# Kernel tuning notes

Hardware: AMD Instinct MI355X
Metric: run time of the kernel (lower is better)

## Reference

```python
import jax, jax.numpy as jnp
import numpy as np

B, N, DIM = 2, 2048, 1024
HEADS, DIM_HEAD = 16, 64
INNER = HEADS * DIM_HEAD  # 1024
SCALE = DIM_HEAD ** -0.5


def setup_inputs() -> dict:
    key = jax.random.key(0)
    ks = jax.random.split(key, 6)
    s = lambda k, shape, fan: jax.random.normal(k, shape, jnp.float32) * (fan ** -0.5)
    return {
        "x": jax.random.normal(ks[0], (B, N, DIM), jnp.float32),
        "similarity": jax.random.normal(ks[1], (B, N), jnp.float32),
        "Wq": s(ks[2], (DIM, INNER), DIM),
        "Wkv": s(ks[3], (DIM, 2 * INNER), DIM),
        "Wo": s(ks[4], (INNER, DIM), INNER),
        "bo": jnp.zeros((DIM,), jnp.float32),
    }


def reference(x, similarity, Wq, Wkv, Wo, bo):
    b, n, _ = x.shape
    h, d = HEADS, DIM_HEAD
    # projections (context = x, self-attention)
    q = (x @ Wq).reshape(b, n, h, d).transpose(0, 2, 1, 3)        # b h n d
    kv = x @ Wkv                                                   # b n 2*inner
    k, v = jnp.split(kv, 2, axis=-1)
    k = k.reshape(b, n, h, d).transpose(0, 2, 1, 3)
    v = v.reshape(b, n, h, d).transpose(0, 2, 1, 3)
    dots = jnp.einsum('bhid,bhjd->bhij', q, k) * SCALE             # b h n n
    # similarity [b,n] -> broadcast as per-query row bias [b,1,n,1]
    dots = dots + similarity[:, None, :, None]
    attn = jax.nn.softmax(dots, axis=-1)
    out = jnp.einsum('bhij,bhjd->bhid', attn, v)                   # b h n d
    out = out.transpose(0, 2, 1, 3).reshape(b, n, h * d)           # b n inner
    return out @ Wo + bo
```

## Files before the change

### kernel.cpp

```cpp
#include <hip/hip_runtime.h>


typedef __attribute__((ext_vector_type(8))) short short8;
typedef __attribute__((ext_vector_type(4))) float float4_;
typedef __attribute__((ext_vector_type(16))) float floatx16;
typedef __attribute__((ext_vector_type(4))) unsigned short ushort4_;
typedef __attribute__((ext_vector_type(4))) unsigned int uint4_;

#define MFMA(a, b, c) __builtin_amdgcn_mfma_f32_16x16x32_bf16((a), (b), (c), 0, 0, 0)
#define MFMA32(a, b, c) __builtin_amdgcn_mfma_f32_32x32x16_bf16((a), (b), (c), 0, 0, 0)

static __device__ __forceinline__ unsigned short f2bf(float f) {
    union { float f; unsigned int u; } v; v.f = f;
    unsigned int r = v.u + 0x7FFFu + ((v.u >> 16) & 1u);
    return (unsigned short)(r >> 16);
}

static __device__ __forceinline__ void gld16(const void* g, void* l) {
    __builtin_amdgcn_global_load_lds(
        (__attribute__((address_space(1))) void*)(g),
        (__attribute__((address_space(3))) void*)(l), 16, 0, 0);
}

__global__ __launch_bounds__(256) void prep(
    const float* __restrict__ X, const float* __restrict__ Wq,
    const float* __restrict__ Wkv, const float* __restrict__ Wo,
    unsigned short* __restrict__ xb, unsigned short* __restrict__ Wt,
    unsigned short* __restrict__ Wot)
{
    const int bid = blockIdx.x, t = threadIdx.x;
    if (bid >= 1024) {
        const int b = bid - 1024;
        const float4_* src = (const float4_*)X;
        ushort4_* dst = (ushort4_*)xb;
        #pragma unroll
        for (int g = 0; g < 8; ++g) {
            const int idx = b * 2048 + g * 256 + t;
            float4_ v = src[idx];
            ushort4_ o;
            o[0] = f2bf(v[0]); o[1] = f2bf(v[1]);
            o[2] = f2bf(v[2]); o[3] = f2bf(v[3]);
            dst[idx] = o;
        }
        return;
    }
    __shared__ float tile[64][65];
    const float* src; unsigned short* dst; int N, kt, nt, drow0;
    if (bid < 256)      { src = Wq;  N = 1024; kt = bid & 15;       nt = bid >> 4;       dst = Wt;  drow0 = nt * 64; }
    else if (bid < 768) { src = Wkv; N = 2048; kt = (bid-256) & 15; nt = (bid-256) >> 4; dst = Wt;  drow0 = 1024 + nt * 64; }
    else                { src = Wo;  N = 1024; kt = (bid-768) & 15; nt = (bid-768) >> 4; dst = Wot; drow0 = nt * 64; }
    const int k0 = kt * 64, n0 = nt * 64;
    const int r0 = t >> 6, c = t & 63;
    #pragma unroll
    for (int i = 0; i < 16; ++i) {
        const int r = i * 4 + r0;
        tile[r][c] = src[(size_t)(k0 + r) * N + n0 + c];
    }
    __syncthreads();
    #pragma unroll
    for (int i = 0; i < 16; ++i) {
        const int rn = i * 4 + r0;
        dst[(size_t)(drow0 + rn) * 1024 + k0 + c] = f2bf(tile[c][rn]);
    }
}

__global__ __launch_bounds__(256) void qkv_gemm2(
    const unsigned short* __restrict__ xb, const unsigned short* __restrict__ Wt,
    unsigned short* __restrict__ q_ws, unsigned short* __restrict__ k_ws,
    unsigned short* __restrict__ vt_ws)
{
    __shared__ unsigned short As[128 * 64];
    __shared__ unsigned short Bs[128 * 64];
    const int t = threadIdx.x, wave = t >> 6, lane = t & 63;
    const int L = lane & 15, quad = lane >> 4;
    const int xcd = blockIdx.x & 7, idx = blockIdx.x >> 3;
    const int mb = (xcd >> 1) * 8 + (idx & 7);
    const int nb = (xcd & 1) * 12 + (idx >> 3);
    const int m0 = mb * 128, n0 = nb * 128;
    const int wr = wave >> 1, wc = wave & 1;

    float4_ z = {0.f, 0.f, 0.f, 0.f};
    float4_ acc[4][4];
    #pragma unroll
    for (int i = 0; i < 4; ++i)
        #pragma unroll
        for (int j = 0; j < 4; ++j) acc[i][j] = z;

    const unsigned short* gA[4]; const unsigned short* gB[4];
    unsigned short* lA[4]; unsigned short* lB[4];
    #pragma unroll
    for (int j = 0; j < 4; ++j) {
        const int cid = wave * 256 + j * 64 + lane;
        const int row = cid >> 3, pc = cid & 7;
        const int lch = pc ^ (row & 7);
        gA[j] = xb + (size_t)(m0 + row) * 1024 + lch * 8;
        gB[j] = Wt + (size_t)(n0 + row) * 1024 + lch * 8;
        lA[j] = As + wave * 2048 + j * 512;
        lB[j] = Bs + wave * 2048 + j * 512;
    }

    for (int kc = 0; kc < 1024; kc += 64) {
        #pragma unroll
        for (int j = 0; j < 4; ++j) {
            gld16(gA[j] + kc, lA[j]);
            gld16(gB[j] + kc, lB[j]);
        }
        __syncthreads();
        #pragma unroll
        for (int ks = 0; ks < 2; ++ks) {
            short8 af[4], bfr[4];
            #pragma unroll
            for (int mt = 0; mt < 4; ++mt) {
                const int rl = wr * 64 + mt * 16 + L;
                af[mt] = *(const short8*)(As + rl * 64 + (((ks * 4 + quad) ^ (L & 7)) << 3));
            }
            #pragma unroll
            for (int nt = 0; nt < 4; ++nt) {
                const int rl = wc * 64 + nt * 16 + L;
                bfr[nt] = *(const short8*)(Bs + rl * 64 + (((ks * 4 + quad) ^ (L & 7)) << 3));
            }
            #pragma unroll
            for (int mt = 0; mt < 4; ++mt)
                #pragma unroll
                for (int nt = 0; nt < 4; ++nt)
                    acc[mt][nt] = MFMA(af[mt], bfr[nt], acc[mt][nt]);
        }
        __syncthreads();
    }

    const int b = m0 >> 11;
    const int type = n0 >> 10;
    #pragma unroll
    for (int mt = 0; mt < 4; ++mt) {
        const int m = (m0 & 2047) + wr * 64 + mt * 16 + quad * 4;
        #pragma unroll
        for (int nt = 0; nt < 4; ++nt) {
            const int cl = (n0 & 1023) + wc * 64 + nt * 16 + L;
            const int h = cl >> 6, d = cl & 63;
            float4_ v = acc[mt][nt];
            if (type == 0) {
                unsigned short* p = q_ws + ((size_t)(b * 16 + h) * 2048 + m) * 64 + d;
                #pragma unroll
                for (int r = 0; r < 4; ++r) p[(size_t)r * 64] = f2bf(v[r] * 0.18033688011f);
            } else if (type == 1) {
                unsigned short* p = k_ws + (size_t)(b * 16 + h) * 131072
                    + (m >> 5) * 2048 + (d >> 3) * 256 + (m & 31) * 8 + (d & 7);
                #pragma unroll
                for (int r = 0; r < 4; ++r) p[r * 8] = f2bf(v[r]);
            } else {
                ushort4_ pk;
                pk[0] = f2bf(v[0]); pk[1] = f2bf(v[1]);
                pk[2] = f2bf(v[2]); pk[3] = f2bf(v[3]);
                *(ushort4_*)(vt_ws + (size_t)(b * 16 + h) * 131072
                    + (m >> 3) * 512 + d * 8 + (m & 7)) = pk;
            }
        }
    }
}

#define LOADT(k0_, k1_, k2_, k3_, v00_, v10_, v01_, v11_, IT) do {            \
    const unsigned short* kp_ = kbase + (IT) * 2048;                          \
    const unsigned short* vp_ = vbase + (IT) * 2048;                          \
    k0_ = *(const short8*)(kp_);        k1_ = *(const short8*)(kp_ + 512);    \
    k2_ = *(const short8*)(kp_ + 1024); k3_ = *(const short8*)(kp_ + 1536);   \
    v00_ = *(const short8*)(vp_);        v10_ = *(const short8*)(vp_ + 1024); \
    v01_ = *(const short8*)(vp_ + 256);  v11_ = *(const short8*)(vp_ + 1280); \
} while (0)

#define COMPT(k0_, k1_, k2_, k3_, v00_, v10_, v01_, v11_) do {                \
    _Pragma("unroll")                                                         \
    for (int qt = 0; qt < 2; ++qt) {                                          \
        floatx16 s;                                                           \
        _Pragma("unroll")                                                     \
        for (int r = 0; r < 16; ++r) s[r] = 0.f;                              \
        s = MFMA32(k0_, qf[qt][0], s);                                        \
        s = MFMA32(k1_, qf[qt][1], s);                                        \
        s = MFMA32(k2_, qf[qt][2], s);                                        \
        s = MFMA32(k3_, qf[qt][3], s);                                        \
        unsigned int pk[8];                                                   \
        float ls_ = 0.f;                                                      \
        _Pragma("unroll")                                                     \
        for (int d = 0; d < 8; ++d) {                                         \
            union { float f; unsigned int u; } a_, b_;                        \
            a_.f = __builtin_amdgcn_exp2f(s[2 * d]);                          \
            b_.f = __builtin_amdgcn_exp2f(s[2 * d + 1]);                      \
            ls_ += a_.f + b_.f;                                               \
            pk[d] = __builtin_amdgcn_perm(b_.u, a_.u, 0x07060302u);           \
        }                                                                     \
        lsum[qt] += ls_;                                                      \
        uint4_ w0_, w1_;                                                      \
        w0_[0] = pk[0]; w0_[1] = pk[1]; w0_[2] = pk[2]; w0_[3] = pk[3];       \
        w1_[0] = pk[4]; w1_[1] = pk[5]; w1_[2] = pk[6]; w1_[3] = pk[7];       \
        short8 pa0 = *(short8*)&w0_, pa1 = *(short8*)&w1_;                    \
        o[qt][0] = MFMA32(pa0, v00_, o[qt][0]);                               \
        o[qt][0] = MFMA32(pa1, v10_, o[qt][0]);                               \
        o[qt][1] = MFMA32(pa0, v01_, o[qt][1]);                               \
        o[qt][1] = MFMA32(pa1, v11_, o[qt][1]);                               \
    }                                                                         \
} while (0)

__global__ __launch_bounds__(128, 2) void attn_fwd7(
    const unsigned short* __restrict__ q_ws,
    const unsigned short* __restrict__ k_ws,
    const unsigned short* __restrict__ vt_ws,
    unsigned short* __restrict__ o2)
{
    __shared__ float cbuf[2][2048];
    __shared__ float lsd[2][2][32];
    const int t = threadIdx.x, wave = t >> 6, lane = t & 63;
    const int l32 = lane & 31, hi = lane >> 5;
    const int xcd = blockIdx.x & 7, loc = blockIdx.x >> 3;
    const int bh = xcd * 4 + (loc >> 5);
    const int qb = loc & 31;

    short8 qf[2][4];
    #pragma unroll
    for (int qt = 0; qt < 2; ++qt) {
        const unsigned short* Qp = q_ws
            + ((size_t)(bh * 2048 + qb * 64 + qt * 32 + l32)) * 64 + hi * 8;
        #pragma unroll
        for (int ks = 0; ks < 4; ++ks)
            qf[qt][ks] = *(const short8*)(Qp + ks * 16);
    }

    const int piRow = (l32 & ~12) | ((l32 & 4) << 1) | ((l32 & 8) >> 1);
    const unsigned short* kbase = k_ws + (size_t)bh * 131072
        + wave * 65536 + hi * 256 + piRow * 8;
    const unsigned short* vbase = vt_ws + (size_t)bh * 131072
        + wave * 65536 + hi * 512 + l32 * 8;

    floatx16 o[2][2];
    float lsum[2] = {0.f, 0.f};
    #pragma unroll
    for (int qt = 0; qt < 2; ++qt)
        #pragma unroll
        for (int r = 0; r < 16; ++r) { o[qt][0][r] = 0.f; o[qt][1][r] = 0.f; }

    short8 kA0, kA1, kA2, kA3, vA00, vA10, vA01, vA11;
    short8 kB0, kB1, kB2, kB3, vB00, vB10, vB01, vB11;
    LOADT(kA0, kA1, kA2, kA3, vA00, vA10, vA01, vA11, 0);

    #pragma unroll 1
    for (int it = 0; it < 32; it += 2) {
        LOADT(kB0, kB1, kB2, kB3, vB00, vB10, vB01, vB11, it + 1);
        COMPT(kA0, kA1, kA2, kA3, vA00, vA10, vA01, vA11);
        LOADT(kA0, kA1, kA2, kA3, vA00, vA10, vA01, vA11, (it + 2) & 31);
        COMPT(kB0, kB1, kB2, kB3, vB00, vB10, vB01, vB11);
    }

    #pragma unroll
    for (int qt = 0; qt < 2; ++qt) {
        float ltot = lsum[qt] + __shfl_xor(lsum[qt], 32);
        lsd[wave][qt][l32] = ltot;
    }

    const int qtd = wave ^ 1;
    float* myb = cbuf[wave];
    #pragma unroll
    for (int r = 0; r < 16; ++r) {
        myb[r * 64 + lane]        = o[qtd][0][r];
        myb[(16 + r) * 64 + lane] = o[qtd][1][r];
    }
    __syncthreads();
    const float* otb = cbuf[wave ^ 1];
    const int qto = wave;
    const int b = bh >> 4, h = bh & 15;
    unsigned short* obase = o2 + ((size_t)(b * 2048 + qb * 64)) * 1024 + h * 64;
    #pragma unroll
    for (int r = 0; r < 16; ++r) {
        const int rowloc = (r & 3) + 8 * (r >> 2) + 4 * hi;
        const float o0v = o[qto][0][r] + otb[r * 64 + lane];
        const float o1v = o[qto][1][r] + otb[(16 + r) * 64 + lane];
        const float iv = 1.0f / (lsd[0][qto][rowloc] + lsd[1][qto][rowloc]);
        const int row = qto * 32 + rowloc;
        obase[(size_t)row * 1024 + l32]      = f2bf(o0v * iv);
        obase[(size_t)row * 1024 + 32 + l32] = f2bf(o1v * iv);
    }
}

__global__ __launch_bounds__(256) void out_gemm2(
    const unsigned short* __restrict__ o2, const unsigned short* __restrict__ Wot,
    const float* __restrict__ bo, float* __restrict__ Out)
{
    __shared__ unsigned short As[128 * 64];
    __shared__ unsigned short Bs[64 * 64];
    const int t = threadIdx.x, wave = t >> 6, lane = t & 63;
    const int L = lane & 15, quad = lane >> 4;
    const int xcd = blockIdx.x & 7, idx = blockIdx.x >> 3;
    const int mb = (xcd >> 1) * 8 + (idx & 7);
    const int nb = (xcd & 1) * 8 + (idx >> 3);
    const int m0 = mb * 128, n0 = nb * 64;
    const int wr = wave >> 1, wc = wave & 1;

    float4_ z = {0.f, 0.f, 0.f, 0.f};
    float4_ acc[4][2];
    #pragma unroll
    for (int i = 0; i < 4; ++i)
        #pragma unroll
        for (int j = 0; j < 2; ++j) acc[i][j] = z;

    const unsigned short* gA[4]; unsigned short* lA[4];
    #pragma unroll
    for (int j = 0; j < 4; ++j) {
        const int cid = wave * 256 + j * 64 + lane;
        const int row = cid >> 3, pc = cid & 7;
        gA[j] = o2 + (size_t)(m0 + row) * 1024 + (pc ^ (row & 7)) * 8;
        lA[j] = As + wave * 2048 + j * 512;
    }
    const unsigned short* gB[2]; unsigned short* lB[2];
    #pragma unroll
    for (int j = 0; j < 2; ++j) {
        const int cid = wave * 128 + j * 64 + lane;
        const int row = cid >> 3, pc = cid & 7;
        gB[j] = Wot + (size_t)(n0 + row) * 1024 + (pc ^ (row & 7)) * 8;
        lB[j] = Bs + wave * 1024 + j * 512;
    }

    for (int kc = 0; kc < 1024; kc += 64) {
        #pragma unroll
        for (int j = 0; j < 4; ++j) gld16(gA[j] + kc, lA[j]);
        #pragma unroll
        for (int j = 0; j < 2; ++j) gld16(gB[j] + kc, lB[j]);
        __syncthreads();
        #pragma unroll
        for (int ks = 0; ks < 2; ++ks) {
            short8 af[4], bfr[2];
            #pragma unroll
            for (int mt = 0; mt < 4; ++mt) {
                const int rl = wr * 64 + mt * 16 + L;
                af[mt] = *(const short8*)(As + rl * 64 + (((ks * 4 + quad) ^ (L & 7)) << 3));
            }
            #pragma unroll
            for (int nt = 0; nt < 2; ++nt) {
                const int rl = wc * 32 + nt * 16 + L;
                bfr[nt] = *(const short8*)(Bs + rl * 64 + (((ks * 4 + quad) ^ (L & 7)) << 3));
            }
            #pragma unroll
            for (int mt = 0; mt < 4; ++mt)
                #pragma unroll
                for (int nt = 0; nt < 2; ++nt)
                    acc[mt][nt] = MFMA(af[mt], bfr[nt], acc[mt][nt]);
        }
        __syncthreads();
    }

    #pragma unroll
    for (int mt = 0; mt < 4; ++mt) {
        const int m = m0 + wr * 64 + mt * 16 + quad * 4;
        #pragma unroll
        for (int nt = 0; nt < 2; ++nt) {
            const int c = n0 + wc * 32 + nt * 16 + L;
            const float bias = bo[c];
            #pragma unroll
            for (int r = 0; r < 4; ++r)
                Out[(size_t)(m + r) * 1024 + c] = acc[mt][nt][r] + bias;
        }
    }
}

extern "C" void kernel_launch(void* const* d_in, const int* in_sizes, int n_in,
                              void* d_out, int out_size, void* d_ws, size_t ws_size,
                              hipStream_t stream) {
    const float* x   = (const float*)d_in[0];
    const float* Wq  = (const float*)d_in[2];
    const float* Wkv = (const float*)d_in[3];
    const float* Wo  = (const float*)d_in[4];
    const float* bo  = (const float*)d_in[5];
    float* out = (float*)d_out;

    char* ws = (char*)d_ws;
    const size_t MB = 1024 * 1024;
    unsigned short* xb   = (unsigned short*)(ws);
    unsigned short* o2   = xb;
    unsigned short* Wt   = (unsigned short*)(ws + 8 * MB);
    unsigned short* Wot  = (unsigned short*)(ws + 14 * MB);
    unsigned short* q_ws = (unsigned short*)(ws + 16 * MB);
    unsigned short* k_ws = (unsigned short*)(ws + 24 * MB);
    unsigned short* vt_ws= (unsigned short*)(ws + 32 * MB);

    prep<<<dim3(1536), dim3(256), 0, stream>>>(x, Wq, Wkv, Wo, xb, Wt, Wot);
    qkv_gemm2<<<dim3(768), dim3(256), 0, stream>>>(xb, Wt, q_ws, k_ws, vt_ws);
    attn_fwd7<<<dim3(1024), dim3(128), 0, stream>>>(q_ws, k_ws, vt_ws, o2);
    out_gemm2<<<dim3(512), dim3(256), 0, stream>>>(o2, Wot, bo, out);
}
```

Before: 195.3 us.

## Split attention query tiles across four waves per block instead of two

The attention kernel now uses 256 threads per block. Each wave handles one 32-row query group and one half of the keys, where before two waves each handled both query groups. This halves per-wave registers (one Q fragment set, two accumulators) so occupancy can rise, with launch bounds going to 3 blocks per CU. The K/V double-buffer prefetch is also restructured so loads are issued two tiles ahead. The cross-wave reduction now writes each key-half partial to LDS and lets the kh==0 waves finalize.

```diff
diff --git a/kernel.cpp b/kernel.cpp
--- a/kernel.cpp
+++ b/kernel.cpp
@@ -158,7 +158,7 @@
     }
 }
 
-#define LOADT(k0_, k1_, k2_, k3_, v00_, v10_, v01_, v11_, IT) do {            \
+#define LOADT13(k0_, k1_, k2_, k3_, v00_, v10_, v01_, v11_, IT) do {          \
     const unsigned short* kp_ = kbase + (IT) * 2048;                          \
     const unsigned short* vp_ = vbase + (IT) * 2048;                          \
     k0_ = *(const short8*)(kp_);        k1_ = *(const short8*)(kp_ + 512);    \
@@ -167,39 +167,34 @@
     v01_ = *(const short8*)(vp_ + 256);  v11_ = *(const short8*)(vp_ + 1280); \
 } while (0)
 
-#define COMPT(k0_, k1_, k2_, k3_, v00_, v10_, v01_, v11_) do {                \
+#define COMPT13(k0_, k1_, k2_, k3_, v00_, v10_, v01_, v11_) do {              \
+    floatx16 s;                                                               \
     _Pragma("unroll")                                                         \
-    for (int qt = 0; qt < 2; ++qt) {                                          \
-        floatx16 s;                                                           \
-        _Pragma("unroll")                                                     \
-        for (int r = 0; r < 16; ++r) s[r] = 0.f;                              \
-        s = MFMA32(k0_, qf[qt][0], s);                                        \
-        s = MFMA32(k1_, qf[qt][1], s);                                        \
-        s = MFMA32(k2_, qf[qt][2], s);                                        \
-        s = MFMA32(k3_, qf[qt][3], s);                                        \
-        unsigned int pk[8];                                                   \
-        float ls_ = 0.f;                                                      \
-        _Pragma("unroll")                                                     \
-        for (int d = 0; d < 8; ++d) {                                         \
-            union { float f; unsigned int u; } a_, b_;                        \
-            a_.f = __builtin_amdgcn_exp2f(s[2 * d]);                          \
-            b_.f = __builtin_amdgcn_exp2f(s[2 * d + 1]);                      \
-            ls_ += a_.f + b_.f;                                               \
-            pk[d] = __builtin_amdgcn_perm(b_.u, a_.u, 0x07060302u);           \
-        }                                                                     \
-        lsum[qt] += ls_;                                                      \
-        uint4_ w0_, w1_;                                                      \
-        w0_[0] = pk[0]; w0_[1] = pk[1]; w0_[2] = pk[2]; w0_[3] = pk[3];       \
-        w1_[0] = pk[4]; w1_[1] = pk[5]; w1_[2] = pk[6]; w1_[3] = pk[7];       \
-        short8 pa0 = *(short8*)&w0_, pa1 = *(short8*)&w1_;                    \
-        o[qt][0] = MFMA32(pa0, v00_, o[qt][0]);                               \
-        o[qt][0] = MFMA32(pa1, v10_, o[qt][0]);                               \
-        o[qt][1] = MFMA32(pa0, v01_, o[qt][1]);                               \
-        o[qt][1] = MFMA32(pa1, v11_, o[qt][1]);                               \
+    for (int r = 0; r < 16; ++r) s[r] = 0.f;                                  \
+    s = MFMA32(k0_, qf[0], s);                                                \
+    s = MFMA32(k1_, qf[1], s);                                                \
+    s = MFMA32(k2_, qf[2], s);                                                \
+    s = MFMA32(k3_, qf[3], s);                                                \
+    unsigned int pk[8];                                                       \
+    _Pragma("unroll")                                                         \
+    for (int d = 0; d < 8; ++d) {                                             \
+        union { float f; unsigned int u; } a_, b_;                            \
+        a_.f = __builtin_amdgcn_exp2f(s[2 * d]);                              \
+        b_.f = __builtin_amdgcn_exp2f(s[2 * d + 1]);                          \
+        lsum += a_.f + b_.f;                                                  \
+        pk[d] = __builtin_amdgcn_perm(b_.u, a_.u, 0x07060302u);               \
     }                                                                         \
+    uint4_ w0_, w1_;                                                          \
+    w0_[0] = pk[0]; w0_[1] = pk[1]; w0_[2] = pk[2]; w0_[3] = pk[3];           \
+    w1_[0] = pk[4]; w1_[1] = pk[5]; w1_[2] = pk[6]; w1_[3] = pk[7];           \
+    short8 pa0 = *(short8*)&w0_, pa1 = *(short8*)&w1_;                        \
+    o0 = MFMA32(pa0, v00_, o0);                                               \
+    o0 = MFMA32(pa1, v10_, o0);                                               \
+    o1 = MFMA32(pa0, v01_, o1);                                               \
+    o1 = MFMA32(pa1, v11_, o1);                                               \
 } while (0)
 
-__global__ __launch_bounds__(128, 2) void attn_fwd7(
+__global__ __launch_bounds__(256, 3) void attn_fwd13(
     const unsigned short* __restrict__ q_ws,
     const unsigned short* __restrict__ k_ws,
     const unsigned short* __restrict__ vt_ws,
@@ -209,72 +204,69 @@
     __shared__ float lsd[2][2][32];
     const int t = threadIdx.x, wave = t >> 6, lane = t & 63;
     const int l32 = lane & 31, hi = lane >> 5;
+    const int qg = wave & 1, kh = wave >> 1;
     const int xcd = blockIdx.x & 7, loc = blockIdx.x >> 3;
     const int bh = xcd * 4 + (loc >> 5);
     const int qb = loc & 31;
 
-    short8 qf[2][4];
-    #pragma unroll
-    for (int qt = 0; qt < 2; ++qt) {
+    short8 qf[4];
+    {
         const unsigned short* Qp = q_ws
-            + ((size_t)(bh * 2048 + qb * 64 + qt * 32 + l32)) * 64 + hi * 8;
-        #pragma unroll
-        for (int ks = 0; ks < 4; ++ks)
-            qf[qt][ks] = *(const short8*)(Qp + ks * 16);
+            + ((size_t)(bh * 2048 + qb * 64 + qg * 32 + l32)) * 64 + hi * 8;
+        #pragma unroll
+        for (int k = 0; k < 4; ++k) qf[k] = *(const short8*)(Qp + k * 16);
     }
 
     const int piRow = (l32 & ~12) | ((l32 & 4) << 1) | ((l32 & 8) >> 1);
     const unsigned short* kbase = k_ws + (size_t)bh * 131072
-        + wave * 65536 + hi * 256 + piRow * 8;
+        + kh * 65536 + hi * 256 + piRow * 8;
     const unsigned short* vbase = vt_ws + (size_t)bh * 131072
-        + wave * 65536 + hi * 512 + l32 * 8;
-
-    floatx16 o[2][2];
-    float lsum[2] = {0.f, 0.f};
-    #pragma unroll
-    for (int qt = 0; qt < 2; ++qt)
-        #pragma unroll
-        for (int r = 0; r < 16; ++r) { o[qt][0][r] = 0.f; o[qt][1][r] = 0.f; }
+        + kh * 65536 + hi * 512 + l32 * 8;
+
+    floatx16 o0, o1;
+    #pragma unroll
+    for (int r = 0; r < 16; ++r) { o0[r] = 0.f; o1[r] = 0.f; }
+    float lsum = 0.f;
 
     short8 kA0, kA1, kA2, kA3, vA00, vA10, vA01, vA11;
     short8 kB0, kB1, kB2, kB3, vB00, vB10, vB01, vB11;
-    LOADT(kA0, kA1, kA2, kA3, vA00, vA10, vA01, vA11, 0);
+    LOADT13(kA0, kA1, kA2, kA3, vA00, vA10, vA01, vA11, 0);
+    LOADT13(kB0, kB1, kB2, kB3, vB00, vB10, vB01, vB11, 1);
 
     #pragma unroll 1
     for (int it = 0; it < 32; it += 2) {
-        LOADT(kB0, kB1, kB2, kB3, vB00, vB10, vB01, vB11, it + 1);
-        COMPT(kA0, kA1, kA2, kA3, vA00, vA10, vA01, vA11);
-        LOADT(kA0, kA1, kA2, kA3, vA00, vA10, vA01, vA11, (it + 2) & 31);
-        COMPT(kB0, kB1, kB2, kB3, vB00, vB10, vB01, vB11);
-    }
-
-    #pragma unroll
-    for (int qt = 0; qt < 2; ++qt) {
-        float ltot = lsum[qt] + __shfl_xor(lsum[qt], 32);
-        lsd[wave][qt][l32] = ltot;
-    }
-
-    const int qtd = wave ^ 1;
-    float* myb = cbuf[wave];
-    #pragma unroll
-    for (int r = 0; r < 16; ++r) {
-        myb[r * 64 + lane]        = o[qtd][0][r];
-        myb[(16 + r) * 64 + lane] = o[qtd][1][r];
+        COMPT13(kA0, kA1, kA2, kA3, vA00, vA10, vA01, vA11);
+        LOADT13(kA0, kA1, kA2, kA3, vA00, vA10, vA01, vA11, (it + 2) & 31);
+        COMPT13(kB0, kB1, kB2, kB3, vB00, vB10, vB01, vB11);
+        LOADT13(kB0, kB1, kB2, kB3, vB00, vB10, vB01, vB11, (it + 3) & 31);
+    }
+
+    const float lt = lsum + __shfl_xor(lsum, 32);
+    lsd[kh][qg][l32] = lt;
+
+    if (kh == 1) {
+        float* base = cbuf[qg];
+        #pragma unroll
+        for (int r = 0; r < 16; ++r) {
+            base[r * 64 + lane]        = o0[r];
+            base[(16 + r) * 64 + lane] = o1[r];
+        }
     }
     __syncthreads();
-    const float* otb = cbuf[wave ^ 1];
-    const int qto = wave;
-    const int b = bh >> 4, h = bh & 15;
-    unsigned short* obase = o2 + ((size_t)(b * 2048 + qb * 64)) * 1024 + h * 64;
-    #pragma unroll
-    for (int r = 0; r < 16; ++r) {
-        const int rowloc = (r & 3) + 8 * (r >> 2) + 4 * hi;
-        const float o0v = o[qto][0][r] + otb[r * 64 + lane];
-        const float o1v = o[qto][1][r] + otb[(16 + r) * 64 + lane];
-        const float iv = 1.0f / (lsd[0][qto][rowloc] + lsd[1][qto][rowloc]);
-        const int row = qto * 32 + rowloc;
-        obase[(size_t)row * 1024 + l32]      = f2bf(o0v * iv);
-        obase[(size_t)row * 1024 + 32 + l32] = f2bf(o1v * iv);
+    if (kh == 0) {
+        const int b = bh >> 4, h = bh & 15;
+        const float* base = cbuf[qg];
+        unsigned short* obase = o2
+            + ((size_t)(b * 2048 + qb * 64 + qg * 32)) * 1024 + h * 64;
+        #pragma unroll
+        for (int r = 0; r < 16; ++r) {
+            const int rowloc = (r & 3) + 8 * (r >> 2) + 4 * hi;
+            const float iv = 1.0f / (lsd[0][qg][rowloc] + lsd[1][qg][rowloc]);
+            const float a0 = o0[r] + base[r * 64 + lane];
+            const float a1 = o1[r] + base[(16 + r) * 64 + lane];
+            obase[(size_t)rowloc * 1024 + l32]      = f2bf(a0 * iv);
+            obase[(size_t)rowloc * 1024 + 32 + l32] = f2bf(a1 * iv);
+        }
     }
 }
 
@@ -380,6 +372,6 @@
 
     prep<<<dim3(1536), dim3(256), 0, stream>>>(x, Wq, Wkv, Wo, xb, Wt, Wot);
     qkv_gemm2<<<dim3(768), dim3(256), 0, stream>>>(xb, Wt, q_ws, k_ws, vt_ws);
-    attn_fwd7<<<dim3(1024), dim3(128), 0, stream>>>(q_ws, k_ws, vt_ws, o2);
+    attn_fwd13<<<dim3(1024), dim3(256), 0, stream>>>(q_ws, k_ws, vt_ws, o2);
     out_gemm2<<<dim3(512), dim3(256), 0, stream>>>(o2, Wot, bo, out);
 }
```

New measurement: 198.2 us. No clear change (+1.5%).
